# Performance work log

Measured on AMD Instinct MI355X. Metric: run time of the kernel, lower is better.

The kernel has to match this reference:

```python
import jax, jax.numpy as jnp
import numpy as np
from jax import lax

B, C, H, W = 16, 3, 256, 256
K = 3          # lbp kernel size (odd)
POOL = 3       # avg pool size (odd so shapes are preserved)
Q = 8          # quant_len


def _build_lbp_kernel():
    mid = K // 2
    idx_pairs = [((0, 0), (K - 1, K - 1)), ((0, mid), (K - 1, mid)),
                 ((0, K - 1), (K - 1, 0)), ((mid, K - 1), (mid, 0))]
    ks = []
    for a, b in idx_pairs:
        for pos in (a, b):
            k = np.zeros((C, K, K), np.float32)
            k[:, mid, mid] = 1.0
            k[:, pos[0], pos[1]] = -1.0
            ks.append(k)
    return jnp.asarray(np.stack(ks))  # [8, C, K, K]

LBP_KERNEL = _build_lbp_kernel()
# cartesian_prod(arange(Q), arange(Q)) -> first coord slowest (row-major)
IDXS = jnp.asarray(np.stack(np.meshgrid(np.arange(Q), np.arange(Q), indexing='ij'), -1)
                   .reshape(Q * Q, 2).astype(np.float32))  # [64, 2]


def _forward(x, w_expand, b_expand, w_conv, b_conv, w_final, b_final, clamp_low, clamp_high):
    b = x.shape[0]
    # avg_pool2d(kernel=POOL, stride=1, pad=POOL//2, count_include_pad=True)
    p = POOL // 2
    xp = jnp.pad(x, ((0, 0), (0, 0), (p, p), (p, p)))
    x = lax.reduce_window(xp, 0.0, lax.add, (1, 1, POOL, POOL), (1, 1, 1, 1), 'VALID') / (POOL * POOL)
    # 8-channel LBP difference conv, 'same' padding
    x = lax.conv_general_dilated(x, LBP_KERNEL, (1, 1), ((K // 2, K // 2), (K // 2, K // 2)),
                                 dimension_numbers=('NCHW', 'OIHW', 'NCHW'))  # [B,8,H,W]
    x = jnp.clip(x, clamp_low[0], clamp_high[0])
    b4 = b * 4
    v = x.reshape(b4, 2, H * W)                    # pairwise channels
    mn = v.min(-1)                                 # [b4,2]
    mx = v.max(-1)
    lev = mn[..., None] + (mx - mn)[..., None] * (jnp.arange(Q, dtype=v.dtype) / Q)  # [b4,2,Q]
    hi = jnp.concatenate([lev[..., 1:], mx[..., None]], -1)                          # [b4,2,Q]
    vq = v[:, :, None, :]                                                            # [b4,2,1,HW]
    # keep value if lev[l] <= v <= hi[l], else 0 (values equal to a boundary land in both bins)
    masked = jnp.where((vq >= lev[..., None]) & (vq <= hi[..., None]), vq, 0.0)      # [b4,2,Q,HW]
    # joint weighted histogram: sum_p v0[p in bin i] * v1[p in bin j]
    hist = jnp.einsum('bip,bjp->bij', masked[:, 0], masked[:, 1])                    # [b4,Q,Q]
    hist = (hist / jnp.sum(hist)).reshape(b4, Q * Q)
    feats = jnp.concatenate([jnp.broadcast_to(IDXS, (b4, Q * Q, 2)), hist[..., None]], -1)  # [b4,64,3]
    f = feats.reshape(b, 4, Q * Q, 3).transpose(0, 3, 1, 2)                          # [B,3,4,64]
    y = jax.nn.leaky_relu(jnp.einsum('bchw,oc->bohw', f, w_expand) + b_expand[None, :, None, None])
    y = y.transpose(0, 2, 3, 1)                                                      # [B,4,64,56]
    # torch nearest interpolate: src = floor(dst * in / out)
    h_in, w_in = y.shape[-2], y.shape[-1]
    rows = (jnp.arange(H) * h_in) // H
    cols = (jnp.arange(W) * w_in) // W
    y = y[:, :, rows][:, :, :, cols]                                                 # [B,4,H,W]
    # layer_norm over last two dims, no affine
    mean = y.mean((-2, -1), keepdims=True)
    var = ((y - mean) ** 2).mean((-2, -1), keepdims=True)
    y = (y - mean) / jnp.sqrt(var + 1e-5)
    y = jax.nn.leaky_relu(jnp.einsum('bchw,oc->bohw', y, w_conv) + b_conv[None, :, None, None])
    y = lax.conv_general_dilated(y, w_final, (1, 1), ((1, 1), (1, 1)),
                                 dimension_numbers=('NCHW', 'OIHW', 'NCHW')) + b_final[None, :, None, None]
    return jax.nn.leaky_relu(y)                                                      # [B,1,H,W]


def setup_inputs() -> dict:
    key = jax.random.key(0)
    ks = jax.random.split(key, 7)
    return {
        'x': jax.random.normal(ks[0], (B, C, H, W), jnp.float32),
        'w_expand': jax.random.normal(ks[1], (56, 3), jnp.float32) * 0.1,
        'b_expand': jax.random.normal(ks[2], (56,), jnp.float32) * 0.1,
        'w_conv': jax.random.normal(ks[3], (16, 4), jnp.float32) * 0.1,
        'b_conv': jax.random.normal(ks[4], (16,), jnp.float32) * 0.1,
        'w_final': jax.random.normal(ks[5], (1, 16, 3, 3), jnp.float32) * 0.1,
        'b_final': jax.random.normal(ks[6], (1,), jnp.float32) * 0.1,
        'clamp_low': jnp.full((1,), -150.0, jnp.float32),
        'clamp_high': jnp.full((1,), 150.0, jnp.float32),
    }


def reference(x, w_expand, b_expand, w_conv, b_conv, w_final, b_final, clamp_low, clamp_high):
    return _forward(x, w_expand, b_expand, w_conv, b_conv, w_final, b_final, clamp_low, clamp_high)
```

## Files before the change

kernel.cpp:

```cpp
#include <hip/hip_runtime.h>
#include <math.h>

#define NB   16
#define HW   65536
#define NCHM 32
#define NCHH 16

#define OFF_S    0
#define OFF_MN   1048576
#define OFF_MX   1048704
#define OFF_HIST 1048832
#define OFF_TOT  1052928
#define OFF_Y1   1052932
#define OFF_PH   1052932
#define OFF_PMN  1118468
#define OFF_PMX  1122564
#define OFF_MEAN 1282308
#define OFF_ISTD 1282372
#define OFF_ZC   0

__device__ __forceinline__ float leakyf(float v) { return v >= 0.f ? v : 0.01f * v; }

__global__ void k_box(const float* __restrict__ x, float* __restrict__ ws)
{
    __shared__ float t[18][20];
    int b  = blockIdx.z;
    int h0 = blockIdx.y * 16, w0 = blockIdx.x * 16;
    int tid = threadIdx.y * 16 + threadIdx.x;
    const float* xb = x + (size_t)b * 3 * HW;
    for (int i = tid; i < 18 * 18; i += 256) {
        int lh = i / 18, lw = i % 18;
        int gh = h0 - 1 + lh, gw = w0 - 1 + lw;
        float v = 0.f;
        if (gh >= 0 && gh < 256 && gw >= 0 && gw < 256) {
            int p = gh * 256 + gw;
            v = xb[p] + xb[HW + p] + xb[2 * HW + p];
        }
        t[lh][lw] = v;
    }
    __syncthreads();
    int ty = threadIdx.y, tx = threadIdx.x;
    float s = 0.f;
    #pragma unroll
    for (int dy = 0; dy < 3; ++dy)
        #pragma unroll
        for (int dx = 0; dx < 3; ++dx)
            s += t[ty + dy][tx + dx];
    ws[OFF_S + b * HW + (h0 + ty) * 256 + (w0 + tx)] = s / 9.0f;
}

__global__ void k_minmax_part(const float* __restrict__ clo, const float* __restrict__ chi,
                              float* ws)
{
    const int doy[8] = {-1, 1, -1, 1, -1, 1, 0, 0};
    const int dox[8] = {-1, 1,  0, 0,  1, -1, 1, -1};
    int b  = blockIdx.x / NCHM;
    int ch = blockIdx.x % NCHM;
    float lo = clo[0], hi = chi[0];
    const float* Sb = ws + OFF_S + b * HW;
    float vmn[8], vmx[8];
    #pragma unroll
    for (int o = 0; o < 8; ++o) { vmn[o] = 3.4e38f; vmx[o] = -3.4e38f; }
    int base = ch * (HW / NCHM);
    #pragma unroll
    for (int it = 0; it < (HW / NCHM) / 256; ++it) {
        int p = base + it * 256 + threadIdx.x;
        int h = p >> 8, w = p & 255;
        float sc = Sb[p];
        #pragma unroll
        for (int o = 0; o < 8; ++o) {
            int nh = h + doy[o], nw = w + dox[o];
            float off = ((unsigned)nh < 256u && (unsigned)nw < 256u) ? Sb[nh * 256 + nw] : 0.f;
            float v = fminf(fmaxf(sc - off, lo), hi);
            vmn[o] = fminf(vmn[o], v);
            vmx[o] = fmaxf(vmx[o], v);
        }
    }
    #pragma unroll
    for (int o = 0; o < 8; ++o) {
        #pragma unroll
        for (int m = 1; m < 64; m <<= 1) {
            vmn[o] = fminf(vmn[o], __shfl_xor(vmn[o], m));
            vmx[o] = fmaxf(vmx[o], __shfl_xor(vmx[o], m));
        }
    }
    __shared__ float smn[4][8], smx[4][8];
    int wid = threadIdx.x >> 6, lane = threadIdx.x & 63;
    if (lane == 0) {
        #pragma unroll
        for (int o = 0; o < 8; ++o) { smn[wid][o] = vmn[o]; smx[wid][o] = vmx[o]; }
    }
    __syncthreads();
    if (threadIdx.x < 8) {
        int o = threadIdx.x;
        float mn = fminf(fminf(smn[0][o], smn[1][o]), fminf(smn[2][o], smn[3][o]));
        float mx = fmaxf(fmaxf(smx[0][o], smx[1][o]), fmaxf(smx[2][o], smx[3][o]));
        ws[OFF_PMN + (b * 8 + o) * NCHM + ch] = mn;
        ws[OFF_PMX + (b * 8 + o) * NCHM + ch] = mx;
    }
}

__global__ void k_minmax_red(float* ws)
{
    int bo = threadIdx.x;
    if (bo < 128) {
        float mn = 3.4e38f, mx = -3.4e38f;
        for (int c = 0; c < NCHM; ++c) {
            mn = fminf(mn, ws[OFF_PMN + bo * NCHM + c]);
            mx = fmaxf(mx, ws[OFF_PMX + bo * NCHM + c]);
        }
        ws[OFF_MN + bo] = mn;
        ws[OFF_MX + bo] = mx;
    }
}

__global__ void k_hist_part(const float* __restrict__ clo, const float* __restrict__ chi,
                            float* ws)
{
    __shared__ float lh[64 * 64];
    const int doy[8] = {-1, 1, -1, 1, -1, 1, 0, 0};
    const int dox[8] = {-1, 1,  0, 0,  1, -1, 1, -1};
    int bg = blockIdx.x / NCHH;
    int ch = blockIdx.x % NCHH;
    int b = bg >> 2, g = bg & 3;
    int dy0 = doy[2 * g], dx0 = dox[2 * g];
    int dy1 = doy[2 * g + 1], dx1 = dox[2 * g + 1];
    float mn0 = ws[OFF_MN + b * 8 + 2 * g],     mx0 = ws[OFF_MX + b * 8 + 2 * g];
    float mn1 = ws[OFF_MN + b * 8 + 2 * g + 1], mx1 = ws[OFF_MX + b * 8 + 2 * g + 1];
    float r0 = mx0 - mn0, r1 = mx1 - mn1;
    float lev0[8], lev1[8];
    #pragma unroll
    for (int q = 0; q < 8; ++q) {
        lev0[q] = __fadd_rn(mn0, __fmul_rn(r0, (float)q * 0.125f));
        lev1[q] = __fadd_rn(mn1, __fmul_rn(r1, (float)q * 0.125f));
    }
    const float* Sb = ws + OFF_S + b * HW;
    for (int i = threadIdx.x; i < 4096; i += 256) lh[i] = 0.f;
    __syncthreads();
    int col = threadIdx.x & 63;
    float lo = clo[0], hi = chi[0];
    int base = ch * (HW / NCHH);
    #pragma unroll
    for (int it = 0; it < (HW / NCHH) / 256; ++it) {
        int p = base + it * 256 + threadIdx.x;
        int h = p >> 8, w = p & 255;
        float off0 = 0.f, off1 = 0.f;
        int nh = h + dy0, nw = w + dx0;
        if ((unsigned)nh < 256u && (unsigned)nw < 256u) off0 = Sb[nh * 256 + nw];
        nh = h + dy1; nw = w + dx1;
        if ((unsigned)nh < 256u && (unsigned)nw < 256u) off1 = Sb[nh * 256 + nw];
        float sc = Sb[p];
        float v0 = fminf(fmaxf(sc - off0, lo), hi);
        float v1 = fminf(fmaxf(sc - off1, lo), hi);
        int i0 = 0, j0 = 0;
        bool ilo = false, jlo = false;
        #pragma unroll
        for (int k = 1; k < 8; ++k) {
            i0 += (v0 >= lev0[k]); ilo |= (v0 == lev0[k]);
            j0 += (v1 >= lev1[k]); jlo |= (v1 == lev1[k]);
        }
        float prod = v0 * v1;
        atomicAdd(&lh[(i0 * 8 + j0) * 64 + col], prod);
        if (ilo)        atomicAdd(&lh[((i0 - 1) * 8 + j0) * 64 + col], prod);
        if (jlo)        atomicAdd(&lh[(i0 * 8 + (j0 - 1)) * 64 + col], prod);
        if (ilo && jlo) atomicAdd(&lh[((i0 - 1) * 8 + (j0 - 1)) * 64 + col], prod);
    }
    __syncthreads();
    if (threadIdx.x < 64) {
        int bin = threadIdx.x;
        float s = 0.f;
        for (int c = 0; c < 64; ++c) s += lh[bin * 64 + ((c + bin) & 63)];
        ws[OFF_PH + blockIdx.x * 64 + bin] = s;
    }
}

__global__ void k_hist_red(float* ws)
{
    int idx = blockIdx.x * 256 + threadIdx.x;
    if (idx < 4096) {
        int bg = idx >> 6, bin = idx & 63;
        float s = 0.f;
        #pragma unroll
        for (int c = 0; c < NCHH; ++c)
            s += ws[OFF_PH + (bg * NCHH + c) * 64 + bin];
        ws[OFF_HIST + idx] = s;
    }
}

__global__ void k_total(float* ws)
{
    __shared__ float sm[256];
    float s = 0.f;
    for (int i = threadIdx.x; i < 4096; i += 256) s += ws[OFF_HIST + i];
    sm[threadIdx.x] = s;
    __syncthreads();
    for (int k = 128; k > 0; k >>= 1) {
        if (threadIdx.x < k) sm[threadIdx.x] += sm[threadIdx.x + k];
        __syncthreads();
    }
    if (threadIdx.x == 0) ws[OFF_TOT] = sm[0];
}

__global__ void k_expand(const float* __restrict__ we, const float* __restrict__ be,
                         float* ws)
{
    int bg = blockIdx.x;
    float total = ws[OFF_TOT];
    float ls = 0.f, lss = 0.f;
    for (int idx = threadIdx.x; idx < 64 * 56; idx += 256) {
        int q = idx / 56, o = idx % 56;
        float fi = (float)(q >> 3), fj = (float)(q & 7);
        float hv = ws[OFF_HIST + bg * 64 + q] / total;
        float y = we[o * 3 + 0] * fi + we[o * 3 + 1] * fj + we[o * 3 + 2] * hv + be[o];
        y = leakyf(y);
        ws[OFF_Y1 + (bg * 64 + q) * 56 + o] = y;
        int cnt = ((32 * (o + 1) + 6) / 7) - ((32 * o + 6) / 7);
        float wgt = (float)(4 * cnt);
        ls  += y * wgt;
        lss += y * y * wgt;
    }
    __shared__ float s1[256], s2[256];
    s1[threadIdx.x] = ls; s2[threadIdx.x] = lss;
    __syncthreads();
    for (int k = 128; k > 0; k >>= 1) {
        if (threadIdx.x < k) { s1[threadIdx.x] += s1[threadIdx.x + k]; s2[threadIdx.x] += s2[threadIdx.x + k]; }
        __syncthreads();
    }
    if (threadIdx.x == 0) {
        float mean = s1[0] / 65536.0f;
        float var  = s2[0] / 65536.0f - mean * mean;
        ws[OFF_MEAN + bg] = mean;
        ws[OFF_ISTD + bg] = 1.0f / sqrtf(var + 1e-5f);
    }
}

__global__ void k_zc(const float* __restrict__ wc, const float* __restrict__ bc, float* ws)
{
    int flat = blockIdx.x * 256 + threadIdx.x;
    int c = flat & 15;
    int rest = flat >> 4;
    int o = rest % 56;
    int rest2 = rest / 56;
    int q = rest2 & 63;
    int b = rest2 >> 6;
    float acc = 0.f;
    #pragma unroll
    for (int g = 0; g < 4; ++g) {
        int bg = b * 4 + g;
        float yn = (ws[OFF_Y1 + (bg * 64 + q) * 56 + o] - ws[OFF_MEAN + bg]) * ws[OFF_ISTD + bg];
        acc += wc[c * 4 + g] * yn;
    }
    ws[OFF_ZC + flat] = leakyf(acc + bc[c]);
}

__global__ void __launch_bounds__(256) k_final(const float* __restrict__ ws,
                                               const float* __restrict__ wf,
                                               const float* __restrict__ bf,
                                               float* __restrict__ out)
{
    __shared__ float swf[144];
    if (threadIdx.x < 144) swf[threadIdx.x] = wf[threadIdx.x];
    __syncthreads();
    int pix = blockIdx.x * 256 + threadIdx.x;
    int wwp = pix & 255, hhp = (pix >> 8) & 255, b = pix >> 16;
    float acc = 0.f;
    #pragma unroll
    for (int kh = 0; kh < 3; ++kh) {
        int h2 = hhp + kh - 1;
        if (h2 < 0 || h2 > 255) continue;
        int qr = h2 >> 2;
        #pragma unroll
        for (int kw = 0; kw < 3; ++kw) {
            int w2 = wwp + kw - 1;
            if (w2 < 0 || w2 > 255) continue;
            int oc = (w2 * 7) >> 5;
            const float* z = ws + OFF_ZC + ((b * 64 + qr) * 56 + oc) * 16;
            #pragma unroll
            for (int c = 0; c < 16; ++c)
                acc += z[c] * swf[c * 9 + kh * 3 + kw];
        }
    }
    out[pix] = leakyf(acc + bf[0]);
}

extern "C" void kernel_launch(void* const* d_in, const int* in_sizes, int n_in,
                              void* d_out, int out_size, void* d_ws, size_t ws_size,
                              hipStream_t stream)
{
    const float* x   = (const float*)d_in[0];
    const float* we  = (const float*)d_in[1];
    const float* be  = (const float*)d_in[2];
    const float* wc  = (const float*)d_in[3];
    const float* bc  = (const float*)d_in[4];
    const float* wf  = (const float*)d_in[5];
    const float* bfi = (const float*)d_in[6];
    const float* clo = (const float*)d_in[7];
    const float* chi = (const float*)d_in[8];
    float* out = (float*)d_out;
    float* ws  = (float*)d_ws;

    dim3 blk(16, 16);
    dim3 grd(16, 16, NB);
    k_box<<<grd, blk, 0, stream>>>(x, ws);
    k_minmax_part<<<NB * NCHM, 256, 0, stream>>>(clo, chi, ws);
    k_minmax_red<<<1, 256, 0, stream>>>(ws);
    k_hist_part<<<64 * NCHH, 256, 0, stream>>>(clo, chi, ws);
    k_hist_red<<<16, 256, 0, stream>>>(ws);
    k_total<<<1, 256, 0, stream>>>(ws);
    k_expand<<<64, 256, 0, stream>>>(we, be, ws);
    k_zc<<<3584, 256, 0, stream>>>(wc, bc, ws);
    k_final<<<4096, 256, 0, stream>>>(ws, wf, bfi, out);
}
```

Before: 158.0 us.

## Fuse histogram reduction, expand, norm, channel mix into one kernel; precompute tap sums

Drops the minmax reduction kernel by having each histogram block reduce the partial min/max itself. Merges the histogram reduction, total, expand, normalisation and channel-mix kernels into one per-batch kernel that keeps intermediates in shared memory. That kernel also folds the 16-channel final conv weights into nine per-tap planes, so the final kernel does only nine loads per pixel. This removes several launches and global round trips. The trade-off is a 16-block fused kernel with low parallelism, where every block redundantly sums all partial histograms to get the global total.

```diff
diff --git a/kernel.cpp b/kernel.cpp
--- a/kernel.cpp
+++ b/kernel.cpp
@@ -7,17 +7,10 @@
 #define NCHH 16
 
 #define OFF_S    0
-#define OFF_MN   1048576
-#define OFF_MX   1048704
-#define OFF_HIST 1048832
-#define OFF_TOT  1052928
-#define OFF_Y1   1052932
-#define OFF_PH   1052932
-#define OFF_PMN  1118468
-#define OFF_PMX  1122564
-#define OFF_MEAN 1282308
-#define OFF_ISTD 1282372
-#define OFF_ZC   0
+#define OFF_D    0
+#define OFF_PH   1048576
+#define OFF_PMN  1114112
+#define OFF_PMX  1118208
 
 __device__ __forceinline__ float leakyf(float v) { return v >= 0.f ? v : 0.01f * v; }
 
@@ -100,20 +93,6 @@
     }
 }
 
-__global__ void k_minmax_red(float* ws)
-{
-    int bo = threadIdx.x;
-    if (bo < 128) {
-        float mn = 3.4e38f, mx = -3.4e38f;
-        for (int c = 0; c < NCHM; ++c) {
-            mn = fminf(mn, ws[OFF_PMN + bo * NCHM + c]);
-            mx = fmaxf(mx, ws[OFF_PMX + bo * NCHM + c]);
-        }
-        ws[OFF_MN + bo] = mn;
-        ws[OFF_MX + bo] = mx;
-    }
-}
-
 __global__ void k_hist_part(const float* __restrict__ clo, const float* __restrict__ chi,
                             float* ws)
 {
@@ -125,8 +104,16 @@
     int b = bg >> 2, g = bg & 3;
     int dy0 = doy[2 * g], dx0 = dox[2 * g];
     int dy1 = doy[2 * g + 1], dx1 = dox[2 * g + 1];
-    float mn0 = ws[OFF_MN + b * 8 + 2 * g],     mx0 = ws[OFF_MX + b * 8 + 2 * g];
-    float mn1 = ws[OFF_MN + b * 8 + 2 * g + 1], mx1 = ws[OFF_MX + b * 8 + 2 * g + 1];
+    float mn0 = 3.4e38f, mx0 = -3.4e38f, mn1 = 3.4e38f, mx1 = -3.4e38f;
+    {
+        int c0 = (b * 8 + 2 * g) * NCHM, c1 = (b * 8 + 2 * g + 1) * NCHM;
+        for (int c = 0; c < NCHM; ++c) {
+            mn0 = fminf(mn0, ws[OFF_PMN + c0 + c]);
+            mx0 = fmaxf(mx0, ws[OFF_PMX + c0 + c]);
+            mn1 = fminf(mn1, ws[OFF_PMN + c1 + c]);
+            mx1 = fmaxf(mx1, ws[OFF_PMX + c1 + c]);
+        }
+    }
     float r0 = mx0 - mn0, r1 = mx1 - mn1;
     float lev0[8], lev1[8];
     #pragma unroll
@@ -174,110 +161,134 @@
     }
 }
 
-__global__ void k_hist_red(float* ws)
-{
-    int idx = blockIdx.x * 256 + threadIdx.x;
-    if (idx < 4096) {
-        int bg = idx >> 6, bin = idx & 63;
+__global__ void __launch_bounds__(256) k_fuse(const float* __restrict__ we,
+                                              const float* __restrict__ be,
+                                              const float* __restrict__ wc,
+                                              const float* __restrict__ bc,
+                                              const float* __restrict__ wf,
+                                              float* ws)
+{
+    __shared__ float shY[4 * 3584];
+    __shared__ float sh_hist[256];
+    __shared__ float sh_red[256];
+    __shared__ float sh_wf[144];
+    __shared__ float sh_we[168];
+    __shared__ float sh_be[56];
+    __shared__ float sh_wc[64];
+    __shared__ float sh_bc[16];
+    __shared__ float sh_stat[8];
+    __shared__ float sw[4][8];
+    __shared__ float sh_tot;
+    int b = blockIdx.x;
+    int tid = threadIdx.x;
+
+    {
+        int g = tid >> 6, bin = tid & 63;
         float s = 0.f;
         #pragma unroll
         for (int c = 0; c < NCHH; ++c)
-            s += ws[OFF_PH + (bg * NCHH + c) * 64 + bin];
-        ws[OFF_HIST + idx] = s;
-    }
-}
-
-__global__ void k_total(float* ws)
-{
-    __shared__ float sm[256];
-    float s = 0.f;
-    for (int i = threadIdx.x; i < 4096; i += 256) s += ws[OFF_HIST + i];
-    sm[threadIdx.x] = s;
+            s += ws[OFF_PH + ((b * 4 + g) * NCHH + c) * 64 + bin];
+        sh_hist[tid] = s;
+    }
+    {
+        float s = 0.f;
+        for (int k = 0; k < 256; ++k)
+            s += ws[OFF_PH + k * 256 + tid];
+        sh_red[tid] = s;
+    }
+    if (tid < 144) sh_wf[tid] = wf[tid];
+    if (tid < 168) sh_we[tid] = we[tid];
+    if (tid < 56)  sh_be[tid] = be[tid];
+    if (tid < 64)  sh_wc[tid] = wc[tid];
+    if (tid < 16)  sh_bc[tid] = bc[tid];
     __syncthreads();
     for (int k = 128; k > 0; k >>= 1) {
-        if (threadIdx.x < k) sm[threadIdx.x] += sm[threadIdx.x + k];
+        if (tid < k) sh_red[tid] += sh_red[tid + k];
         __syncthreads();
     }
-    if (threadIdx.x == 0) ws[OFF_TOT] = sm[0];
-}
-
-__global__ void k_expand(const float* __restrict__ we, const float* __restrict__ be,
-                         float* ws)
-{
-    int bg = blockIdx.x;
-    float total = ws[OFF_TOT];
-    float ls = 0.f, lss = 0.f;
-    for (int idx = threadIdx.x; idx < 64 * 56; idx += 256) {
-        int q = idx / 56, o = idx % 56;
-        float fi = (float)(q >> 3), fj = (float)(q & 7);
-        float hv = ws[OFF_HIST + bg * 64 + q] / total;
-        float y = we[o * 3 + 0] * fi + we[o * 3 + 1] * fj + we[o * 3 + 2] * hv + be[o];
+    if (tid == 0) sh_tot = sh_red[0];
+    __syncthreads();
+    float total = sh_tot;
+
+    float ls[4] = {0.f, 0.f, 0.f, 0.f}, lss[4] = {0.f, 0.f, 0.f, 0.f};
+    for (int it = 0; it < 56; ++it) {
+        int g = it / 14;
+        int rem = (it % 14) * 256 + tid;
+        int q = rem / 56, o = rem % 56;
+        float hv = sh_hist[g * 64 + q] / total;
+        float y = sh_we[o * 3 + 0] * (float)(q >> 3)
+                + sh_we[o * 3 + 1] * (float)(q & 7)
+                + sh_we[o * 3 + 2] * hv + sh_be[o];
         y = leakyf(y);
-        ws[OFF_Y1 + (bg * 64 + q) * 56 + o] = y;
+        shY[g * 3584 + rem] = y;
         int cnt = ((32 * (o + 1) + 6) / 7) - ((32 * o + 6) / 7);
         float wgt = (float)(4 * cnt);
-        ls  += y * wgt;
-        lss += y * y * wgt;
-    }
-    __shared__ float s1[256], s2[256];
-    s1[threadIdx.x] = ls; s2[threadIdx.x] = lss;
-    __syncthreads();
-    for (int k = 128; k > 0; k >>= 1) {
-        if (threadIdx.x < k) { s1[threadIdx.x] += s1[threadIdx.x + k]; s2[threadIdx.x] += s2[threadIdx.x + k]; }
-        __syncthreads();
-    }
-    if (threadIdx.x == 0) {
-        float mean = s1[0] / 65536.0f;
-        float var  = s2[0] / 65536.0f - mean * mean;
-        ws[OFF_MEAN + bg] = mean;
-        ws[OFF_ISTD + bg] = 1.0f / sqrtf(var + 1e-5f);
-    }
-}
-
-__global__ void k_zc(const float* __restrict__ wc, const float* __restrict__ bc, float* ws)
-{
-    int flat = blockIdx.x * 256 + threadIdx.x;
-    int c = flat & 15;
-    int rest = flat >> 4;
-    int o = rest % 56;
-    int rest2 = rest / 56;
-    int q = rest2 & 63;
-    int b = rest2 >> 6;
-    float acc = 0.f;
+        ls[g]  += y * wgt;
+        lss[g] += y * y * wgt;
+    }
     #pragma unroll
     for (int g = 0; g < 4; ++g) {
-        int bg = b * 4 + g;
-        float yn = (ws[OFF_Y1 + (bg * 64 + q) * 56 + o] - ws[OFF_MEAN + bg]) * ws[OFF_ISTD + bg];
-        acc += wc[c * 4 + g] * yn;
-    }
-    ws[OFF_ZC + flat] = leakyf(acc + bc[c]);
+        #pragma unroll
+        for (int m = 1; m < 64; m <<= 1) {
+            ls[g]  += __shfl_xor(ls[g], m);
+            lss[g] += __shfl_xor(lss[g], m);
+        }
+    }
+    int wid = tid >> 6, lane = tid & 63;
+    if (lane == 0) {
+        #pragma unroll
+        for (int g = 0; g < 4; ++g) { sw[wid][g] = ls[g]; sw[wid][4 + g] = lss[g]; }
+    }
+    __syncthreads();
+    if (tid < 4) {
+        float m  = (sw[0][tid] + sw[1][tid] + sw[2][tid] + sw[3][tid]) / 65536.f;
+        float sq = (sw[0][4 + tid] + sw[1][4 + tid] + sw[2][4 + tid] + sw[3][4 + tid]) / 65536.f;
+        sh_stat[tid] = m;
+        sh_stat[4 + tid] = 1.f / sqrtf(sq - m * m + 1e-5f);
+    }
+    __syncthreads();
+
+    for (int it = 0; it < 14; ++it) {
+        int rem = it * 256 + tid;
+        float yn[4];
+        #pragma unroll
+        for (int g = 0; g < 4; ++g)
+            yn[g] = (shY[g * 3584 + rem] - sh_stat[g]) * sh_stat[4 + g];
+        float d[9] = {0.f, 0.f, 0.f, 0.f, 0.f, 0.f, 0.f, 0.f, 0.f};
+        #pragma unroll
+        for (int c = 0; c < 16; ++c) {
+            float z = sh_bc[c];
+            #pragma unroll
+            for (int g = 0; g < 4; ++g) z += sh_wc[c * 4 + g] * yn[g];
+            z = leakyf(z);
+            #pragma unroll
+            for (int t = 0; t < 9; ++t) d[t] += z * sh_wf[c * 9 + t];
+        }
+        #pragma unroll
+        for (int t = 0; t < 9; ++t)
+            ws[OFF_D + (b * 9 + t) * 3584 + rem] = d[t];
+    }
 }
 
 __global__ void __launch_bounds__(256) k_final(const float* __restrict__ ws,
-                                               const float* __restrict__ wf,
                                                const float* __restrict__ bf,
                                                float* __restrict__ out)
 {
-    __shared__ float swf[144];
-    if (threadIdx.x < 144) swf[threadIdx.x] = wf[threadIdx.x];
-    __syncthreads();
     int pix = blockIdx.x * 256 + threadIdx.x;
-    int wwp = pix & 255, hhp = (pix >> 8) & 255, b = pix >> 16;
+    int w = pix & 255, h = (pix >> 8) & 255, b = pix >> 16;
+    const float* Db = ws + OFF_D + b * 9 * 3584;
     float acc = 0.f;
     #pragma unroll
     for (int kh = 0; kh < 3; ++kh) {
-        int h2 = hhp + kh - 1;
-        if (h2 < 0 || h2 > 255) continue;
+        int h2 = h + kh - 1;
+        if ((unsigned)h2 > 255u) continue;
         int qr = h2 >> 2;
         #pragma unroll
         for (int kw = 0; kw < 3; ++kw) {
-            int w2 = wwp + kw - 1;
-            if (w2 < 0 || w2 > 255) continue;
+            int w2 = w + kw - 1;
+            if ((unsigned)w2 > 255u) continue;
             int oc = (w2 * 7) >> 5;
-            const float* z = ws + OFF_ZC + ((b * 64 + qr) * 56 + oc) * 16;
-            #pragma unroll
-            for (int c = 0; c < 16; ++c)
-                acc += z[c] * swf[c * 9 + kh * 3 + kw];
+            acc += Db[(kh * 3 + kw) * 3584 + qr * 56 + oc];
         }
     }
     out[pix] = leakyf(acc + bf[0]);
@@ -303,11 +314,7 @@
     dim3 grd(16, 16, NB);
     k_box<<<grd, blk, 0, stream>>>(x, ws);
     k_minmax_part<<<NB * NCHM, 256, 0, stream>>>(clo, chi, ws);
-    k_minmax_red<<<1, 256, 0, stream>>>(ws);
     k_hist_part<<<64 * NCHH, 256, 0, stream>>>(clo, chi, ws);
-    k_hist_red<<<16, 256, 0, stream>>>(ws);
-    k_total<<<1, 256, 0, stream>>>(ws);
-    k_expand<<<64, 256, 0, stream>>>(we, be, ws);
-    k_zc<<<3584, 256, 0, stream>>>(wc, bc, ws);
-    k_final<<<4096, 256, 0, stream>>>(ws, wf, bfi, out);
-}
+    k_fuse<<<NB, 256, 0, stream>>>(we, be, wc, bc, wf, ws);
+    k_final<<<4096, 256, 0, stream>>>(ws, bfi, out);
+}
```

Measured after the change: 159.8 us. About the same (+1.2%).
